# Performance work log

Measured on AMD Instinct MI355X. Metric: run time of the kernel, lower is better.

## Reference

```python
import jax, jax.numpy as jnp
import numpy as np

# pywt db2 decomposition filters
DEC_LO = np.array([-0.12940952255092145, 0.22414386804185735,
                   0.8365163037378079, 0.4829629131445341], dtype=np.float32)
DEC_HI = np.array([-0.4829629131445341, 0.8365163037378079,
                   -0.22414386804185735, -0.12940952255092145], dtype=np.float32)
LEVEL = 3
REC_WEIGHT = 1.0
FILT_LEN = 4
PAD = (2 * FILT_LEN - 3) // 2  # = 2, ptwt reflect padding per side


def _filters(dtype):
    # ptwt uses cross-correlation with flipped pywt filters (== true convolution)
    lo = jnp.asarray(DEC_LO[::-1].copy(), dtype=dtype)
    hi = jnp.asarray(DEC_HI[::-1].copy(), dtype=dtype)
    ll = jnp.outer(lo, lo)  # 'a'
    lh = jnp.outer(hi, lo)  # 'h'
    hl = jnp.outer(lo, hi)  # 'v'
    hh = jnp.outer(hi, hi)  # 'd'
    return jnp.stack([ll, lh, hl, hh])[:, None]  # [4,1,4,4]


def _dwt_step(x, filt):
    # x: [N, nb, H, W] -> [N, 4*nb, H', W'] (each band split into a,h,v,d; grouped)
    n, nb, h, w = x.shape
    padb = PAD + (h % 2)
    padr = PAD + (w % 2)
    xp = jnp.pad(x, ((0, 0), (0, 0), (PAD, padb), (PAD, padr)), mode='reflect')
    k = jnp.tile(filt, (nb, 1, 1, 1))  # [4*nb, 1, 4, 4]
    return jax.lax.conv_general_dilated(
        xp, k, window_strides=(2, 2), padding='VALID',
        feature_group_count=nb,
        dimension_numbers=('NCHW', 'OIHW', 'NCHW'))


def setup_inputs() -> dict:
    key = jax.random.key(0)
    k1, k2 = jax.random.split(key)
    preds = jax.random.normal(k1, (64, 3, 512, 512), dtype=jnp.float32)
    targets = jax.random.normal(k2, (64, 3, 512, 512), dtype=jnp.float32)
    return {"preds": preds, "targets": targets}


def reference(preds, targets):
    n, c, h, w = preds.shape
    p = preds.reshape(n * c, 1, h, w)
    t = targets.reshape(n * c, 1, h, w)
    filt = _filters(preds.dtype)
    for _ in range(LEVEL):
        p = _dwt_step(p, filt)
        t = _dwt_step(t, filt)
    # p, t: [N*C, 4**LEVEL, h', w']; leaf 0 is the all-'a' (pure approx) packet
    per_leaf_mse = jnp.mean((p - t) ** 2, axis=(0, 2, 3))  # [4**LEVEL]
    wvec = jnp.ones(per_leaf_mse.shape[0], dtype=preds.dtype).at[0].set(0.5)
    return REC_WEIGHT * jnp.dot(wvec, per_leaf_mse)
```

## Files before the change

kernel.cpp:

```cpp
#include <hip/hip_runtime.h>

#define F_LO0 0.4829629131445341f
#define F_LO1 0.8365163037378079f
#define F_LO2 0.22414386804185735f
#define F_LO3 (-0.12940952255092145f)
#define F_HI0 (-0.12940952255092145f)
#define F_HI1 (-0.22414386804185735f)
#define F_HI2 0.8365163037378079f
#define F_HI3 (-0.4829629131445341f)

__device__ __forceinline__ int reflect_idx(int r, int n) {
    r = (r < 0) ? -r : r;
    r = (r >= n) ? 2 * n - 2 - r : r;
    return r;
}

__device__ __forceinline__ float4 vfilt(const float4 a, const float4 b,
                                        const float4 c, const float4 d,
                                        float c0, float c1, float c2, float c3) {
    return make_float4(c0 * a.x + c1 * b.x + c2 * c.x + c3 * d.x,
                       c0 * a.y + c1 * b.y + c2 * c.y + c3 * d.y,
                       c0 * a.z + c1 * b.z + c2 * c.z + c3 * d.z,
                       c0 * a.w + c1 * b.w + c2 * c.w + c3 * d.w);
}

__global__ void __launch_bounds__(512, 6) k_wpt_fused(
    const float* __restrict__ p, const float* __restrict__ t,
    float* __restrict__ partial) {
    constexpr int N0 = 512, N1 = 257, N2 = 130, N3 = 66;

    __shared__ __align__(16) float sA[6080];
    __shared__ __align__(16) float sB[6912];
    __shared__ float wsum[8];

    int bid = blockIdx.x;
    int swz = (bid & 7) * (int)(gridDim.x >> 3) + (bid >> 3);
    int img = swz / 81;
    int tt = swz - img * 81;
    int TA = (tt / 9) * 8;
    int TB = (tt % 9) * 8;

    const int tid = threadIdx.x;
    const size_t ibase = (size_t)img * (N0 * N0);

    const int O0r = 8 * TA - 14, O0c = 8 * TB - 16;
    const int O1r = 4 * TA - 6, O1c = 4 * TB - 6;
    const int O2r = 2 * TA - 2, O2c = 2 * TB - 2;
    const bool edge = (TA == 0) || (TA == 64) || (TB == 0) || (TB == 64);

    if (tid < 390) {
        unsigned ru = (unsigned)tid / 5u;
        const int r = (int)ru;
        const int k = tid - (int)(5u * ru);
        const int grr = reflect_idx(O0r + r, N0);
        const float* __restrict__ prow = p + ibase + (size_t)grr * N0;
        const float* __restrict__ trow = t + ibase + (size_t)grr * N0;
        const int gc0 = O0c + 16 * k;
        float v[20];
        if ((unsigned)gc0 <= 492u) {
#pragma unroll
            for (int q = 0; q < 5; ++q) {
                const float4 pv = *(const float4*)(prow + gc0 + 4 * q);
                const float4 tv = *(const float4*)(trow + gc0 + 4 * q);
                v[4 * q + 0] = pv.x - tv.x;
                v[4 * q + 1] = pv.y - tv.y;
                v[4 * q + 2] = pv.z - tv.z;
                v[4 * q + 3] = pv.w - tv.w;
            }
        } else {
#pragma unroll
            for (int x = 0; x < 20; ++x) {
                int gc = reflect_idx(gc0 + x, N0);
                v[x] = prow[gc] - trow[gc];
            }
        }
        float* dst = sB + r * 40 + 8 * k;
        *(float4*)(dst) = make_float4(
            F_LO0 * v[2] + F_LO1 * v[3] + F_LO2 * v[4] + F_LO3 * v[5],
            F_LO0 * v[4] + F_LO1 * v[5] + F_LO2 * v[6] + F_LO3 * v[7],
            F_LO0 * v[6] + F_LO1 * v[7] + F_LO2 * v[8] + F_LO3 * v[9],
            F_LO0 * v[8] + F_LO1 * v[9] + F_LO2 * v[10] + F_LO3 * v[11]);
        *(float4*)(dst + 4) = make_float4(
            F_LO0 * v[10] + F_LO1 * v[11] + F_LO2 * v[12] + F_LO3 * v[13],
            F_LO0 * v[12] + F_LO1 * v[13] + F_LO2 * v[14] + F_LO3 * v[15],
            F_LO0 * v[14] + F_LO1 * v[15] + F_LO2 * v[16] + F_LO3 * v[17],
            F_LO0 * v[16] + F_LO1 * v[17] + F_LO2 * v[18] + F_LO3 * v[19]);
        *(float4*)(dst + 3120) = make_float4(
            F_HI0 * v[2] + F_HI1 * v[3] + F_HI2 * v[4] + F_HI3 * v[5],
            F_HI0 * v[4] + F_HI1 * v[5] + F_HI2 * v[6] + F_HI3 * v[7],
            F_HI0 * v[6] + F_HI1 * v[7] + F_HI2 * v[8] + F_HI3 * v[9],
            F_HI0 * v[8] + F_HI1 * v[9] + F_HI2 * v[10] + F_HI3 * v[11]);
        *(float4*)(dst + 3124) = make_float4(
            F_HI0 * v[10] + F_HI1 * v[11] + F_HI2 * v[12] + F_HI3 * v[13],
            F_HI0 * v[12] + F_HI1 * v[13] + F_HI2 * v[14] + F_HI3 * v[15],
            F_HI0 * v[14] + F_HI1 * v[15] + F_HI2 * v[16] + F_HI3 * v[17],
            F_HI0 * v[16] + F_HI1 * v[17] + F_HI2 * v[18] + F_HI3 * v[19]);
    }
    __syncthreads();

    if (tid < 380) {
        int r1 = tid / 10, k = tid - r1 * 10;
        const float* blo = sB + (2 * r1) * 40 + 4 * k;
        const float* bhi = blo + 3120;
        float4 L0 = *(const float4*)(blo);
        float4 L1v = *(const float4*)(blo + 40);
        float4 L2v = *(const float4*)(blo + 80);
        float4 L3v = *(const float4*)(blo + 120);
        float4 H0 = *(const float4*)(bhi);
        float4 H1 = *(const float4*)(bhi + 40);
        float4 H2 = *(const float4*)(bhi + 80);
        float4 H3 = *(const float4*)(bhi + 120);
        float4 b0 = vfilt(L0, L1v, L2v, L3v, F_LO0, F_LO1, F_LO2, F_LO3);
        float4 b1 = vfilt(L0, L1v, L2v, L3v, F_HI0, F_HI1, F_HI2, F_HI3);
        float4 b2 = vfilt(H0, H1, H2, H3, F_LO0, F_LO1, F_LO2, F_LO3);
        float4 b3 = vfilt(H0, H1, H2, H3, F_HI0, F_HI1, F_HI2, F_HI3);
        int wo = r1 * 40 + 4 * k;
        *(float4*)(sA + wo) = b0;
        *(float4*)(sA + 1520 + wo) = b1;
        *(float4*)(sA + 3040 + wo) = b2;
        *(float4*)(sA + 4560 + wo) = b3;
    }
    __syncthreads();
    if (edge) {
#pragma unroll
        for (int it = 0; it < 3; ++it) {
            int e = it * 512 + tid;
            if (e < 1444) {
                int lr = e / 38, lc = e - lr * 38;
                int sr = reflect_idx(O1r + lr, N1) - O1r;
                int sc = reflect_idx(O1c + lc, N1) - O1c;
                if ((sr != lr || sc != lc) && (unsigned)sr < 38u && (unsigned)sc < 38u) {
                    int da = lr * 40 + lc;
                    int sa = sr * 40 + sc;
                    sA[da] = sA[sa];
                    sA[1520 + da] = sA[1520 + sa];
                    sA[3040 + da] = sA[3040 + sa];
                    sA[4560 + da] = sA[4560 + sa];
                }
            }
        }
        __syncthreads();
    }

    const int w = tid >> 6;
    const int ln = tid & 63;
    const int bnd = w >> 1;
    const int hf = w & 1;
    const int off = hf * 6;
    float* scr = sB + w * 864;
    const float* L1b = sA + bnd * 1520;

    if (ln < 54) {
        const int c = ln % 18, s = ln / 18;
#pragma unroll
        for (int tq = 0; tq < 4; ++tq) {
            const int r2l = 3 * tq + s;
            const float* base = L1b + (2 * (off + r2l)) * 40 + 2 * c;
            float lo[4], hi[4];
#pragma unroll
            for (int u = 0; u < 4; ++u) {
                float2 a = *(const float2*)(base + u * 40);
                float2 d = *(const float2*)(base + u * 40 + 2);
                lo[u] = F_LO0 * a.x + F_LO1 * a.y + F_LO2 * d.x + F_LO3 * d.y;
                hi[u] = F_HI0 * a.x + F_HI1 * a.y + F_HI2 * d.x + F_HI3 * d.y;
            }
            int sl = r2l * 18 + c;
            scr[sl]       = F_LO0 * lo[0] + F_LO1 * lo[1] + F_LO2 * lo[2] + F_LO3 * lo[3];
            scr[sl + 216] = F_HI0 * lo[0] + F_HI1 * lo[1] + F_HI2 * lo[2] + F_HI3 * lo[3];
            scr[sl + 432] = F_LO0 * hi[0] + F_LO1 * hi[1] + F_LO2 * hi[2] + F_LO3 * hi[3];
            scr[sl + 648] = F_HI0 * hi[0] + F_HI1 * hi[1] + F_HI2 * hi[2] + F_HI3 * hi[3];
        }
    }

    if (edge) {
#pragma unroll
        for (int q = 0; q < 4; ++q) {
            int e = q * 54 + ln;
            if (ln < 54 && e < 216) {
                int lr = e / 18, lc = e - lr * 18;
                int srt = reflect_idx(O2r + off + lr, N2) - O2r - off;
                int sct = reflect_idx(O2c + lc, N2) - O2c;
                if ((srt != lr || sct != lc) &&
                    (unsigned)srt < 12u && (unsigned)sct < 18u) {
                    int d = lr * 18 + lc, sidx = srt * 18 + sct;
#pragma unroll
                    for (int pl = 0; pl < 4; ++pl)
                        scr[d + 216 * pl] = scr[sidx + 216 * pl];
                }
            }
        }
    }

    float local = 0.f;
    {
        const int pp = ln >> 5, rem = ln & 31, r3 = rem >> 3, j = rem & 7;
        const int i = hf * 4 + r3;
        const int sr0 = 2 * r3 + hf * 2;
        const bool valid = (TA + i < N3) && (TB + j < N3);
#pragma unroll
        for (int pi = 0; pi < 2; ++pi) {
            const int pl = 2 * pp + pi;
            const float* pb = scr + pl * 216 + sr0 * 18 + 2 * j;
            float lo[4], hi[4];
#pragma unroll
            for (int u = 0; u < 4; ++u) {
                float2 a = *(const float2*)(pb + u * 18);
                float2 d = *(const float2*)(pb + u * 18 + 2);
                lo[u] = F_LO0 * a.x + F_LO1 * a.y + F_LO2 * d.x + F_LO3 * d.y;
                hi[u] = F_HI0 * a.x + F_HI1 * a.y + F_HI2 * d.x + F_HI3 * d.y;
            }
            float o0 = F_LO0 * lo[0] + F_LO1 * lo[1] + F_LO2 * lo[2] + F_LO3 * lo[3];
            float o1 = F_HI0 * lo[0] + F_HI1 * lo[1] + F_HI2 * lo[2] + F_HI3 * lo[3];
            float o2 = F_LO0 * hi[0] + F_LO1 * hi[1] + F_LO2 * hi[2] + F_LO3 * hi[3];
            float o3 = F_HI0 * hi[0] + F_HI1 * hi[1] + F_HI2 * hi[2] + F_HI3 * hi[3];
            if (valid) {
                float w00 = (bnd == 0 && pl == 0) ? 0.5f : 1.0f;
                local += w00 * o0 * o0 + o1 * o1 + o2 * o2 + o3 * o3;
            }
        }
    }

#pragma unroll
    for (int o = 32; o > 0; o >>= 1) local += __shfl_down(local, o, 64);
    if (ln == 0) wsum[w] = local;
    __syncthreads();
    if (tid == 0) {
        float ssum = 0.f;
#pragma unroll
        for (int x = 0; x < 8; ++x) ssum += wsum[x];
        partial[blockIdx.x] = ssum;
    }
}

__global__ void __launch_bounds__(1024) k_reduce(const float* __restrict__ part,
                                                 float* __restrict__ out,
                                                 int n4, float inv_den) {
    const int tid = threadIdx.x;
    float s = 0.f;
    const float4* p4 = (const float4*)part;
    for (int i = tid; i < n4; i += 1024) {
        float4 v = p4[i];
        s += v.x + v.y + v.z + v.w;
    }
#pragma unroll
    for (int o = 32; o > 0; o >>= 1) s += __shfl_down(s, o, 64);
    __shared__ float ws_[16];
    int w = tid >> 6;
    if ((tid & 63) == 0) ws_[w] = s;
    __syncthreads();
    if (tid == 0) {
        float tot = 0.f;
#pragma unroll
        for (int i = 0; i < 16; ++i) tot += ws_[i];
        out[0] = tot * inv_den;
    }
}

extern "C" void kernel_launch(void* const* d_in, const int* in_sizes, int n_in,
                              void* d_out, int out_size, void* d_ws, size_t ws_size,
                              hipStream_t stream) {
    const float* preds = (const float*)d_in[0];
    const float* targets = (const float*)d_in[1];
    float* out = (float*)d_out;
    float* partial = (float*)d_ws;

    const float inv_den = 1.0f / (192.0f * 66.0f * 66.0f);
    const int nblk = 192 * 9 * 9;

    k_wpt_fused<<<dim3(nblk), dim3(512), 0, stream>>>(preds, targets, partial);
    k_reduce<<<dim3(1), dim3(1024), 0, stream>>>(partial, out, nblk / 4, inv_den);
}
```

Before: 205.2 us.

## Fuse level-1 row/column filtering from global memory and halve LDS scratch

```diff
diff --git a/kernel.cpp b/kernel.cpp
--- a/kernel.cpp
+++ b/kernel.cpp
@@ -15,22 +15,13 @@
     return r;
 }
 
-__device__ __forceinline__ float4 vfilt(const float4 a, const float4 b,
-                                        const float4 c, const float4 d,
-                                        float c0, float c1, float c2, float c3) {
-    return make_float4(c0 * a.x + c1 * b.x + c2 * c.x + c3 * d.x,
-                       c0 * a.y + c1 * b.y + c2 * c.y + c3 * d.y,
-                       c0 * a.z + c1 * b.z + c2 * c.z + c3 * d.z,
-                       c0 * a.w + c1 * b.w + c2 * c.w + c3 * d.w);
-}
-
-__global__ void __launch_bounds__(512, 6) k_wpt_fused(
+__global__ void __launch_bounds__(512, 8) k_wpt_fused(
     const float* __restrict__ p, const float* __restrict__ t,
     float* __restrict__ partial) {
     constexpr int N0 = 512, N1 = 257, N2 = 130, N3 = 66;
 
     __shared__ __align__(16) float sA[6080];
-    __shared__ __align__(16) float sB[6912];
+    __shared__ __align__(16) float sB[3456];
     __shared__ float wsum[8];
 
     int bid = blockIdx.x;
@@ -48,77 +39,59 @@
     const int O2r = 2 * TA - 2, O2c = 2 * TB - 2;
     const bool edge = (TA == 0) || (TA == 64) || (TB == 0) || (TB == 64);
 
-    if (tid < 390) {
-        unsigned ru = (unsigned)tid / 5u;
-        const int r = (int)ru;
-        const int k = tid - (int)(5u * ru);
-        const int grr = reflect_idx(O0r + r, N0);
-        const float* __restrict__ prow = p + ibase + (size_t)grr * N0;
-        const float* __restrict__ trow = t + ibase + (size_t)grr * N0;
-        const int gc0 = O0c + 16 * k;
-        float v[20];
-        if ((unsigned)gc0 <= 492u) {
-#pragma unroll
-            for (int q = 0; q < 5; ++q) {
-                const float4 pv = *(const float4*)(prow + gc0 + 4 * q);
-                const float4 tv = *(const float4*)(trow + gc0 + 4 * q);
-                v[4 * q + 0] = pv.x - tv.x;
-                v[4 * q + 1] = pv.y - tv.y;
-                v[4 * q + 2] = pv.z - tv.z;
-                v[4 * q + 3] = pv.w - tv.w;
-            }
-        } else {
-#pragma unroll
-            for (int x = 0; x < 20; ++x) {
-                int gc = reflect_idx(gc0 + x, N0);
-                v[x] = prow[gc] - trow[gc];
-            }
-        }
-        float* dst = sB + r * 40 + 8 * k;
-        *(float4*)(dst) = make_float4(
-            F_LO0 * v[2] + F_LO1 * v[3] + F_LO2 * v[4] + F_LO3 * v[5],
-            F_LO0 * v[4] + F_LO1 * v[5] + F_LO2 * v[6] + F_LO3 * v[7],
-            F_LO0 * v[6] + F_LO1 * v[7] + F_LO2 * v[8] + F_LO3 * v[9],
-            F_LO0 * v[8] + F_LO1 * v[9] + F_LO2 * v[10] + F_LO3 * v[11]);
-        *(float4*)(dst + 4) = make_float4(
-            F_LO0 * v[10] + F_LO1 * v[11] + F_LO2 * v[12] + F_LO3 * v[13],
-            F_LO0 * v[12] + F_LO1 * v[13] + F_LO2 * v[14] + F_LO3 * v[15],
-            F_LO0 * v[14] + F_LO1 * v[15] + F_LO2 * v[16] + F_LO3 * v[17],
-            F_LO0 * v[16] + F_LO1 * v[17] + F_LO2 * v[18] + F_LO3 * v[19]);
-        *(float4*)(dst + 3120) = make_float4(
-            F_HI0 * v[2] + F_HI1 * v[3] + F_HI2 * v[4] + F_HI3 * v[5],
-            F_HI0 * v[4] + F_HI1 * v[5] + F_HI2 * v[6] + F_HI3 * v[7],
-            F_HI0 * v[6] + F_HI1 * v[7] + F_HI2 * v[8] + F_HI3 * v[9],
-            F_HI0 * v[8] + F_HI1 * v[9] + F_HI2 * v[10] + F_HI3 * v[11]);
-        *(float4*)(dst + 3124) = make_float4(
-            F_HI0 * v[10] + F_HI1 * v[11] + F_HI2 * v[12] + F_HI3 * v[13],
-            F_HI0 * v[12] + F_HI1 * v[13] + F_HI2 * v[14] + F_HI3 * v[15],
-            F_HI0 * v[14] + F_HI1 * v[15] + F_HI2 * v[16] + F_HI3 * v[17],
-            F_HI0 * v[16] + F_HI1 * v[17] + F_HI2 * v[18] + F_HI3 * v[19]);
-    }
-    __syncthreads();
-
     if (tid < 380) {
-        int r1 = tid / 10, k = tid - r1 * 10;
-        const float* blo = sB + (2 * r1) * 40 + 4 * k;
-        const float* bhi = blo + 3120;
-        float4 L0 = *(const float4*)(blo);
-        float4 L1v = *(const float4*)(blo + 40);
-        float4 L2v = *(const float4*)(blo + 80);
-        float4 L3v = *(const float4*)(blo + 120);
-        float4 H0 = *(const float4*)(bhi);
-        float4 H1 = *(const float4*)(bhi + 40);
-        float4 H2 = *(const float4*)(bhi + 80);
-        float4 H3 = *(const float4*)(bhi + 120);
-        float4 b0 = vfilt(L0, L1v, L2v, L3v, F_LO0, F_LO1, F_LO2, F_LO3);
-        float4 b1 = vfilt(L0, L1v, L2v, L3v, F_HI0, F_HI1, F_HI2, F_HI3);
-        float4 b2 = vfilt(H0, H1, H2, H3, F_LO0, F_LO1, F_LO2, F_LO3);
-        float4 b3 = vfilt(H0, H1, H2, H3, F_HI0, F_HI1, F_HI2, F_HI3);
-        int wo = r1 * 40 + 4 * k;
-        *(float4*)(sA + wo) = b0;
-        *(float4*)(sA + 1520 + wo) = b1;
-        *(float4*)(sA + 3040 + wo) = b2;
-        *(float4*)(sA + 4560 + wo) = b3;
+        const int r1 = tid / 10, k = tid - (tid / 10) * 10;
+        const int A = O0c + 8 * k;
+        const bool vec = ((unsigned)A <= 504u);
+        const int q2 = (A <= 500) ? 8 : 4;
+        float b0[4] = {0.f, 0.f, 0.f, 0.f}, b1[4] = {0.f, 0.f, 0.f, 0.f};
+        float b2[4] = {0.f, 0.f, 0.f, 0.f}, b3[4] = {0.f, 0.f, 0.f, 0.f};
+#pragma unroll
+        for (int u = 0; u < 4; ++u) {
+            const int gr = reflect_idx(O0r + 2 * r1 + u, N0);
+            const float* __restrict__ pr = p + ibase + (size_t)gr * N0;
+            const float* __restrict__ tr = t + ibase + (size_t)gr * N0;
+            float v[12];
+            if (vec) {
+                const float4 p0 = *(const float4*)(pr + A);
+                const float4 p1 = *(const float4*)(pr + A + 4);
+                const float4 p2 = *(const float4*)(pr + A + q2);
+                const float4 t0 = *(const float4*)(tr + A);
+                const float4 t1 = *(const float4*)(tr + A + 4);
+                const float4 t2 = *(const float4*)(tr + A + q2);
+                v[0] = p0.x - t0.x; v[1] = p0.y - t0.y; v[2] = p0.z - t0.z; v[3] = p0.w - t0.w;
+                v[4] = p1.x - t1.x; v[5] = p1.y - t1.y; v[6] = p1.z - t1.z; v[7] = p1.w - t1.w;
+                v[8] = p2.x - t2.x; v[9] = p2.y - t2.y; v[10] = p2.z - t2.z; v[11] = p2.w - t2.w;
+            } else {
+#pragma unroll
+                for (int x = 0; x < 12; ++x) {
+                    int gc = reflect_idx(A + x, N0);
+                    v[x] = pr[gc] - tr[gc];
+                }
+            }
+            float lo[4], hi[4];
+#pragma unroll
+            for (int d = 0; d < 4; ++d) {
+                lo[d] = F_LO0 * v[2 * d + 2] + F_LO1 * v[2 * d + 3] +
+                        F_LO2 * v[2 * d + 4] + F_LO3 * v[2 * d + 5];
+                hi[d] = F_HI0 * v[2 * d + 2] + F_HI1 * v[2 * d + 3] +
+                        F_HI2 * v[2 * d + 4] + F_HI3 * v[2 * d + 5];
+            }
+            const float cl = (u == 0) ? F_LO0 : (u == 1) ? F_LO1 : (u == 2) ? F_LO2 : F_LO3;
+            const float ch = (u == 0) ? F_HI0 : (u == 1) ? F_HI1 : (u == 2) ? F_HI2 : F_HI3;
+#pragma unroll
+            for (int d = 0; d < 4; ++d) {
+                b0[d] += cl * lo[d];
+                b1[d] += ch * lo[d];
+                b2[d] += cl * hi[d];
+                b3[d] += ch * hi[d];
+            }
+        }
+        const int wo = r1 * 40 + 4 * k;
+        *(float4*)(sA + wo) = make_float4(b0[0], b0[1], b0[2], b0[3]);
+        *(float4*)(sA + 1520 + wo) = make_float4(b1[0], b1[1], b1[2], b1[3]);
+        *(float4*)(sA + 3040 + wo) = make_float4(b2[0], b2[1], b2[2], b2[3]);
+        *(float4*)(sA + 4560 + wo) = make_float4(b3[0], b3[1], b3[2], b3[3]);
     }
     __syncthreads();
     if (edge) {
@@ -147,60 +120,55 @@
     const int bnd = w >> 1;
     const int hf = w & 1;
     const int off = hf * 6;
-    float* scr = sB + w * 864;
+    float* scr = sB + w * 432;
     const float* L1b = sA + bnd * 1520;
 
-    if (ln < 54) {
-        const int c = ln % 18, s = ln / 18;
-#pragma unroll
-        for (int tq = 0; tq < 4; ++tq) {
-            const int r2l = 3 * tq + s;
-            const float* base = L1b + (2 * (off + r2l)) * 40 + 2 * c;
-            float lo[4], hi[4];
-#pragma unroll
-            for (int u = 0; u < 4; ++u) {
-                float2 a = *(const float2*)(base + u * 40);
-                float2 d = *(const float2*)(base + u * 40 + 2);
-                lo[u] = F_LO0 * a.x + F_LO1 * a.y + F_LO2 * d.x + F_LO3 * d.y;
-                hi[u] = F_HI0 * a.x + F_HI1 * a.y + F_HI2 * d.x + F_HI3 * d.y;
-            }
-            int sl = r2l * 18 + c;
-            scr[sl]       = F_LO0 * lo[0] + F_LO1 * lo[1] + F_LO2 * lo[2] + F_LO3 * lo[3];
-            scr[sl + 216] = F_HI0 * lo[0] + F_HI1 * lo[1] + F_HI2 * lo[2] + F_HI3 * lo[3];
-            scr[sl + 432] = F_LO0 * hi[0] + F_LO1 * hi[1] + F_LO2 * hi[2] + F_LO3 * hi[3];
-            scr[sl + 648] = F_HI0 * hi[0] + F_HI1 * hi[1] + F_HI2 * hi[2] + F_HI3 * hi[3];
-        }
-    }
-
-    if (edge) {
-#pragma unroll
-        for (int q = 0; q < 4; ++q) {
-            int e = q * 54 + ln;
-            if (ln < 54 && e < 216) {
-                int lr = e / 18, lc = e - lr * 18;
-                int srt = reflect_idx(O2r + off + lr, N2) - O2r - off;
-                int sct = reflect_idx(O2c + lc, N2) - O2c;
-                if ((srt != lr || sct != lc) &&
-                    (unsigned)srt < 12u && (unsigned)sct < 18u) {
-                    int d = lr * 18 + lc, sidx = srt * 18 + sct;
-#pragma unroll
-                    for (int pl = 0; pl < 4; ++pl)
-                        scr[d + 216 * pl] = scr[sidx + 216 * pl];
-                }
-            }
-        }
-    }
-
     float local = 0.f;
-    {
-        const int pp = ln >> 5, rem = ln & 31, r3 = rem >> 3, j = rem & 7;
-        const int i = hf * 4 + r3;
-        const int sr0 = 2 * r3 + hf * 2;
-        const bool valid = (TA + i < N3) && (TB + j < N3);
-#pragma unroll
-        for (int pi = 0; pi < 2; ++pi) {
-            const int pl = 2 * pp + pi;
-            const float* pb = scr + pl * 216 + sr0 * 18 + 2 * j;
+#pragma unroll
+    for (int pass = 0; pass < 2; ++pass) {
+        if (ln < 54) {
+            const int c = ln % 18, s = ln / 18;
+#pragma unroll
+            for (int tq = 0; tq < 4; ++tq) {
+                const int r2l = 3 * tq + s;
+                const float* base = L1b + (2 * (off + r2l)) * 40 + 2 * c;
+                float f[4];
+#pragma unroll
+                for (int u = 0; u < 4; ++u) {
+                    float2 a = *(const float2*)(base + u * 40);
+                    float2 d = *(const float2*)(base + u * 40 + 2);
+                    f[u] = (pass == 0)
+                        ? F_LO0 * a.x + F_LO1 * a.y + F_LO2 * d.x + F_LO3 * d.y
+                        : F_HI0 * a.x + F_HI1 * a.y + F_HI2 * d.x + F_HI3 * d.y;
+                }
+                int sl = r2l * 18 + c;
+                scr[sl]       = F_LO0 * f[0] + F_LO1 * f[1] + F_LO2 * f[2] + F_LO3 * f[3];
+                scr[sl + 216] = F_HI0 * f[0] + F_HI1 * f[1] + F_HI2 * f[2] + F_HI3 * f[3];
+            }
+        }
+        if (edge) {
+#pragma unroll
+            for (int q = 0; q < 4; ++q) {
+                int e = q * 54 + ln;
+                if (ln < 54 && e < 216) {
+                    int lr = e / 18, lc = e - lr * 18;
+                    int srt = reflect_idx(O2r + off + lr, N2) - O2r - off;
+                    int sct = reflect_idx(O2c + lc, N2) - O2c;
+                    if ((srt != lr || sct != lc) &&
+                        (unsigned)srt < 12u && (unsigned)sct < 18u) {
+                        int d = lr * 18 + lc, sidx = srt * 18 + sct;
+                        scr[d] = scr[sidx];
+                        scr[d + 216] = scr[sidx + 216];
+                    }
+                }
+            }
+        }
+        {
+            const int pp = ln >> 5, rem = ln & 31, r3 = rem >> 3, j = rem & 7;
+            const int i = hf * 4 + r3;
+            const int sr0 = 2 * r3 + hf * 2;
+            const bool valid = (TA + i < N3) && (TB + j < N3);
+            const float* pb = scr + pp * 216 + sr0 * 18 + 2 * j;
             float lo[4], hi[4];
 #pragma unroll
             for (int u = 0; u < 4; ++u) {
@@ -214,7 +182,7 @@
             float o2 = F_LO0 * hi[0] + F_LO1 * hi[1] + F_LO2 * hi[2] + F_LO3 * hi[3];
             float o3 = F_HI0 * hi[0] + F_HI1 * hi[1] + F_HI2 * hi[2] + F_HI3 * hi[3];
             if (valid) {
-                float w00 = (bnd == 0 && pl == 0) ? 0.5f : 1.0f;
+                float w00 = (bnd == 0 && pass == 0 && pp == 0) ? 0.5f : 1.0f;
                 local += w00 * o0 * o0 + o1 * o1 + o2 * o2 + o3 * o3;
             }
         }
```

Result: slower. 560.7 us (+173.3%).

## Convert fused wavelet kernel to persistent blocks with register prefetch of next tile

Applied to the files above, without the earlier changes.

```diff
diff --git a/kernel.cpp b/kernel.cpp
--- a/kernel.cpp
+++ b/kernel.cpp
@@ -15,6 +15,12 @@
     return r;
 }
 
+#define BARRIER()                                              \
+    do {                                                       \
+        asm volatile("s_waitcnt lgkmcnt(0)" ::: "memory");     \
+        __builtin_amdgcn_s_barrier();                          \
+    } while (0)
+
 __device__ __forceinline__ float4 vfilt(const float4 a, const float4 b,
                                         const float4 c, const float4 d,
                                         float c0, float c1, float c2, float c3) {
@@ -24,7 +30,7 @@
                        c0 * a.w + c1 * b.w + c2 * c.w + c3 * d.w);
 }
 
-__global__ void __launch_bounds__(512, 6) k_wpt_fused(
+__global__ void __launch_bounds__(512) k_wpt_persist(
     const float* __restrict__ p, const float* __restrict__ t,
     float* __restrict__ partial) {
     constexpr int N0 = 512, N1 = 257, N2 = 130, N3 = 66;
@@ -33,191 +39,210 @@
     __shared__ __align__(16) float sB[6912];
     __shared__ float wsum[8];
 
-    int bid = blockIdx.x;
-    int swz = (bid & 7) * (int)(gridDim.x >> 3) + (bid >> 3);
-    int img = swz / 81;
-    int tt = swz - img * 81;
-    int TA = (tt / 9) * 8;
-    int TB = (tt % 9) * 8;
+    const int b = blockIdx.x;
+    const int g0 = b * 30 + ((b < 192) ? b : 192);
+    const int cnt = 30 + ((b < 192) ? 1 : 0);
 
     const int tid = threadIdx.x;
-    const size_t ibase = (size_t)img * (N0 * N0);
-
-    const int O0r = 8 * TA - 14, O0c = 8 * TB - 16;
-    const int O1r = 4 * TA - 6, O1c = 4 * TB - 6;
-    const int O2r = 2 * TA - 2, O2c = 2 * TB - 2;
-    const bool edge = (TA == 0) || (TA == 64) || (TB == 0) || (TB == 64);
-
-    if (tid < 390) {
-        unsigned ru = (unsigned)tid / 5u;
-        const int r = (int)ru;
-        const int k = tid - (int)(5u * ru);
-        const int grr = reflect_idx(O0r + r, N0);
-        const float* __restrict__ prow = p + ibase + (size_t)grr * N0;
-        const float* __restrict__ trow = t + ibase + (size_t)grr * N0;
-        const int gc0 = O0c + 16 * k;
-        float v[20];
+    const int hr = tid / 5, hk = tid - (tid / 5) * 5;
+
+    float4 P[5], T[5];
+
+    auto prefetch = [&](int g) {
+        int img = g / 81;
+        int tt = g - img * 81;
+        int TAn = (tt / 9) * 8;
+        int TBn = (tt - (tt / 9) * 9) * 8;
+        int O0rn = 8 * TAn - 14, O0cn = 8 * TBn - 16;
+        int grr = reflect_idx(O0rn + hr, N0);
+        const float* __restrict__ prow = p + (size_t)img * (N0 * N0) + (size_t)grr * N0;
+        const float* __restrict__ trow = t + (size_t)img * (N0 * N0) + (size_t)grr * N0;
+        int gc0 = O0cn + 16 * hk;
         if ((unsigned)gc0 <= 492u) {
 #pragma unroll
             for (int q = 0; q < 5; ++q) {
-                const float4 pv = *(const float4*)(prow + gc0 + 4 * q);
-                const float4 tv = *(const float4*)(trow + gc0 + 4 * q);
-                v[4 * q + 0] = pv.x - tv.x;
-                v[4 * q + 1] = pv.y - tv.y;
-                v[4 * q + 2] = pv.z - tv.z;
-                v[4 * q + 3] = pv.w - tv.w;
+                P[q] = *(const float4*)(prow + gc0 + 4 * q);
+                T[q] = *(const float4*)(trow + gc0 + 4 * q);
             }
         } else {
 #pragma unroll
-            for (int x = 0; x < 20; ++x) {
-                int gc = reflect_idx(gc0 + x, N0);
-                v[x] = prow[gc] - trow[gc];
-            }
-        }
-        float* dst = sB + r * 40 + 8 * k;
-        *(float4*)(dst) = make_float4(
-            F_LO0 * v[2] + F_LO1 * v[3] + F_LO2 * v[4] + F_LO3 * v[5],
-            F_LO0 * v[4] + F_LO1 * v[5] + F_LO2 * v[6] + F_LO3 * v[7],
-            F_LO0 * v[6] + F_LO1 * v[7] + F_LO2 * v[8] + F_LO3 * v[9],
-            F_LO0 * v[8] + F_LO1 * v[9] + F_LO2 * v[10] + F_LO3 * v[11]);
-        *(float4*)(dst + 4) = make_float4(
-            F_LO0 * v[10] + F_LO1 * v[11] + F_LO2 * v[12] + F_LO3 * v[13],
-            F_LO0 * v[12] + F_LO1 * v[13] + F_LO2 * v[14] + F_LO3 * v[15],
-            F_LO0 * v[14] + F_LO1 * v[15] + F_LO2 * v[16] + F_LO3 * v[17],
-            F_LO0 * v[16] + F_LO1 * v[17] + F_LO2 * v[18] + F_LO3 * v[19]);
-        *(float4*)(dst + 3120) = make_float4(
-            F_HI0 * v[2] + F_HI1 * v[3] + F_HI2 * v[4] + F_HI3 * v[5],
-            F_HI0 * v[4] + F_HI1 * v[5] + F_HI2 * v[6] + F_HI3 * v[7],
-            F_HI0 * v[6] + F_HI1 * v[7] + F_HI2 * v[8] + F_HI3 * v[9],
-            F_HI0 * v[8] + F_HI1 * v[9] + F_HI2 * v[10] + F_HI3 * v[11]);
-        *(float4*)(dst + 3124) = make_float4(
-            F_HI0 * v[10] + F_HI1 * v[11] + F_HI2 * v[12] + F_HI3 * v[13],
-            F_HI0 * v[12] + F_HI1 * v[13] + F_HI2 * v[14] + F_HI3 * v[15],
-            F_HI0 * v[14] + F_HI1 * v[15] + F_HI2 * v[16] + F_HI3 * v[17],
-            F_HI0 * v[16] + F_HI1 * v[17] + F_HI2 * v[18] + F_HI3 * v[19]);
-    }
-    __syncthreads();
-
-    if (tid < 380) {
-        int r1 = tid / 10, k = tid - r1 * 10;
-        const float* blo = sB + (2 * r1) * 40 + 4 * k;
-        const float* bhi = blo + 3120;
-        float4 L0 = *(const float4*)(blo);
-        float4 L1v = *(const float4*)(blo + 40);
-        float4 L2v = *(const float4*)(blo + 80);
-        float4 L3v = *(const float4*)(blo + 120);
-        float4 H0 = *(const float4*)(bhi);
-        float4 H1 = *(const float4*)(bhi + 40);
-        float4 H2 = *(const float4*)(bhi + 80);
-        float4 H3 = *(const float4*)(bhi + 120);
-        float4 b0 = vfilt(L0, L1v, L2v, L3v, F_LO0, F_LO1, F_LO2, F_LO3);
-        float4 b1 = vfilt(L0, L1v, L2v, L3v, F_HI0, F_HI1, F_HI2, F_HI3);
-        float4 b2 = vfilt(H0, H1, H2, H3, F_LO0, F_LO1, F_LO2, F_LO3);
-        float4 b3 = vfilt(H0, H1, H2, H3, F_HI0, F_HI1, F_HI2, F_HI3);
-        int wo = r1 * 40 + 4 * k;
-        *(float4*)(sA + wo) = b0;
-        *(float4*)(sA + 1520 + wo) = b1;
-        *(float4*)(sA + 3040 + wo) = b2;
-        *(float4*)(sA + 4560 + wo) = b3;
-    }
-    __syncthreads();
-    if (edge) {
-#pragma unroll
-        for (int it = 0; it < 3; ++it) {
-            int e = it * 512 + tid;
-            if (e < 1444) {
-                int lr = e / 38, lc = e - lr * 38;
-                int sr = reflect_idx(O1r + lr, N1) - O1r;
-                int sc = reflect_idx(O1c + lc, N1) - O1c;
-                if ((sr != lr || sc != lc) && (unsigned)sr < 38u && (unsigned)sc < 38u) {
-                    int da = lr * 40 + lc;
-                    int sa = sr * 40 + sc;
-                    sA[da] = sA[sa];
-                    sA[1520 + da] = sA[1520 + sa];
-                    sA[3040 + da] = sA[3040 + sa];
-                    sA[4560 + da] = sA[4560 + sa];
-                }
-            }
-        }
-        __syncthreads();
-    }
-
+            for (int q = 0; q < 5; ++q) {
+                int c0 = reflect_idx(gc0 + 4 * q + 0, N0);
+                int c1 = reflect_idx(gc0 + 4 * q + 1, N0);
+                int c2 = reflect_idx(gc0 + 4 * q + 2, N0);
+                int c3 = reflect_idx(gc0 + 4 * q + 3, N0);
+                P[q] = make_float4(prow[c0], prow[c1], prow[c2], prow[c3]);
+                T[q] = make_float4(trow[c0], trow[c1], trow[c2], trow[c3]);
+            }
+        }
+    };
+
+    if (tid < 390) prefetch(g0);
+
+    float local = 0.f;
     const int w = tid >> 6;
     const int ln = tid & 63;
     const int bnd = w >> 1;
     const int hf = w & 1;
     const int off = hf * 6;
     float* scr = sB + w * 864;
-    const float* L1b = sA + bnd * 1520;
-
-    if (ln < 54) {
-        const int c = ln % 18, s = ln / 18;
-#pragma unroll
-        for (int tq = 0; tq < 4; ++tq) {
-            const int r2l = 3 * tq + s;
-            const float* base = L1b + (2 * (off + r2l)) * 40 + 2 * c;
-            float lo[4], hi[4];
-#pragma unroll
-            for (int u = 0; u < 4; ++u) {
-                float2 a = *(const float2*)(base + u * 40);
-                float2 d = *(const float2*)(base + u * 40 + 2);
-                lo[u] = F_LO0 * a.x + F_LO1 * a.y + F_LO2 * d.x + F_LO3 * d.y;
-                hi[u] = F_HI0 * a.x + F_HI1 * a.y + F_HI2 * d.x + F_HI3 * d.y;
-            }
-            int sl = r2l * 18 + c;
-            scr[sl]       = F_LO0 * lo[0] + F_LO1 * lo[1] + F_LO2 * lo[2] + F_LO3 * lo[3];
-            scr[sl + 216] = F_HI0 * lo[0] + F_HI1 * lo[1] + F_HI2 * lo[2] + F_HI3 * lo[3];
-            scr[sl + 432] = F_LO0 * hi[0] + F_LO1 * hi[1] + F_LO2 * hi[2] + F_LO3 * hi[3];
-            scr[sl + 648] = F_HI0 * hi[0] + F_HI1 * hi[1] + F_HI2 * hi[2] + F_HI3 * hi[3];
-        }
-    }
-
-    if (edge) {
-#pragma unroll
-        for (int q = 0; q < 4; ++q) {
-            int e = q * 54 + ln;
-            if (ln < 54 && e < 216) {
-                int lr = e / 18, lc = e - lr * 18;
-                int srt = reflect_idx(O2r + off + lr, N2) - O2r - off;
-                int sct = reflect_idx(O2c + lc, N2) - O2c;
-                if ((srt != lr || sct != lc) &&
-                    (unsigned)srt < 12u && (unsigned)sct < 18u) {
-                    int d = lr * 18 + lc, sidx = srt * 18 + sct;
-#pragma unroll
-                    for (int pl = 0; pl < 4; ++pl)
-                        scr[d + 216 * pl] = scr[sidx + 216 * pl];
-                }
-            }
-        }
-    }
-
-    float local = 0.f;
-    {
-        const int pp = ln >> 5, rem = ln & 31, r3 = rem >> 3, j = rem & 7;
-        const int i = hf * 4 + r3;
-        const int sr0 = 2 * r3 + hf * 2;
-        const bool valid = (TA + i < N3) && (TB + j < N3);
-#pragma unroll
-        for (int pi = 0; pi < 2; ++pi) {
-            const int pl = 2 * pp + pi;
-            const float* pb = scr + pl * 216 + sr0 * 18 + 2 * j;
-            float lo[4], hi[4];
-#pragma unroll
-            for (int u = 0; u < 4; ++u) {
-                float2 a = *(const float2*)(pb + u * 18);
-                float2 d = *(const float2*)(pb + u * 18 + 2);
-                lo[u] = F_LO0 * a.x + F_LO1 * a.y + F_LO2 * d.x + F_LO3 * d.y;
-                hi[u] = F_HI0 * a.x + F_HI1 * a.y + F_HI2 * d.x + F_HI3 * d.y;
-            }
-            float o0 = F_LO0 * lo[0] + F_LO1 * lo[1] + F_LO2 * lo[2] + F_LO3 * lo[3];
-            float o1 = F_HI0 * lo[0] + F_HI1 * lo[1] + F_HI2 * lo[2] + F_HI3 * lo[3];
-            float o2 = F_LO0 * hi[0] + F_LO1 * hi[1] + F_LO2 * hi[2] + F_LO3 * hi[3];
-            float o3 = F_HI0 * hi[0] + F_HI1 * hi[1] + F_HI2 * hi[2] + F_HI3 * hi[3];
-            if (valid) {
-                float w00 = (bnd == 0 && pl == 0) ? 0.5f : 1.0f;
-                local += w00 * o0 * o0 + o1 * o1 + o2 * o2 + o3 * o3;
-            }
-        }
+
+    for (int it = 0; it < cnt; ++it) {
+        const int g = g0 + it;
+        const int img = g / 81;
+        const int tt = g - img * 81;
+        const int TA = (tt / 9) * 8;
+        const int TB = (tt - (tt / 9) * 9) * 8;
+        const int O1r = 4 * TA - 6, O1c = 4 * TB - 6;
+        const int O2r = 2 * TA - 2, O2c = 2 * TB - 2;
+        const bool edge = (TA == 0) || (TA == 64) || (TB == 0) || (TB == 64);
+
+        if (tid < 390) {
+            float v[20];
+#pragma unroll
+            for (int q = 0; q < 5; ++q) {
+                v[4 * q + 0] = P[q].x - T[q].x;
+                v[4 * q + 1] = P[q].y - T[q].y;
+                v[4 * q + 2] = P[q].z - T[q].z;
+                v[4 * q + 3] = P[q].w - T[q].w;
+            }
+            if (it + 1 < cnt) prefetch(g + 1);
+            float* dst = sB + hr * 40 + 8 * hk;
+            *(float4*)(dst) = make_float4(
+                F_LO0 * v[2] + F_LO1 * v[3] + F_LO2 * v[4] + F_LO3 * v[5],
+                F_LO0 * v[4] + F_LO1 * v[5] + F_LO2 * v[6] + F_LO3 * v[7],
+                F_LO0 * v[6] + F_LO1 * v[7] + F_LO2 * v[8] + F_LO3 * v[9],
+                F_LO0 * v[8] + F_LO1 * v[9] + F_LO2 * v[10] + F_LO3 * v[11]);
+            *(float4*)(dst + 4) = make_float4(
+                F_LO0 * v[10] + F_LO1 * v[11] + F_LO2 * v[12] + F_LO3 * v[13],
+                F_LO0 * v[12] + F_LO1 * v[13] + F_LO2 * v[14] + F_LO3 * v[15],
+                F_LO0 * v[14] + F_LO1 * v[15] + F_LO2 * v[16] + F_LO3 * v[17],
+                F_LO0 * v[16] + F_LO1 * v[17] + F_LO2 * v[18] + F_LO3 * v[19]);
+            *(float4*)(dst + 3120) = make_float4(
+                F_HI0 * v[2] + F_HI1 * v[3] + F_HI2 * v[4] + F_HI3 * v[5],
+                F_HI0 * v[4] + F_HI1 * v[5] + F_HI2 * v[6] + F_HI3 * v[7],
+                F_HI0 * v[6] + F_HI1 * v[7] + F_HI2 * v[8] + F_HI3 * v[9],
+                F_HI0 * v[8] + F_HI1 * v[9] + F_HI2 * v[10] + F_HI3 * v[11]);
+            *(float4*)(dst + 3124) = make_float4(
+                F_HI0 * v[10] + F_HI1 * v[11] + F_HI2 * v[12] + F_HI3 * v[13],
+                F_HI0 * v[12] + F_HI1 * v[13] + F_HI2 * v[14] + F_HI3 * v[15],
+                F_HI0 * v[14] + F_HI1 * v[15] + F_HI2 * v[16] + F_HI3 * v[17],
+                F_HI0 * v[16] + F_HI1 * v[17] + F_HI2 * v[18] + F_HI3 * v[19]);
+        }
+        BARRIER();
+
+        if (tid < 380) {
+            int r1 = tid / 10, k = tid - (tid / 10) * 10;
+            const float* blo = sB + (2 * r1) * 40 + 4 * k;
+            const float* bhi = blo + 3120;
+            float4 L0 = *(const float4*)(blo);
+            float4 L1v = *(const float4*)(blo + 40);
+            float4 L2v = *(const float4*)(blo + 80);
+            float4 L3v = *(const float4*)(blo + 120);
+            float4 H0 = *(const float4*)(bhi);
+            float4 H1 = *(const float4*)(bhi + 40);
+            float4 H2 = *(const float4*)(bhi + 80);
+            float4 H3 = *(const float4*)(bhi + 120);
+            float4 b0 = vfilt(L0, L1v, L2v, L3v, F_LO0, F_LO1, F_LO2, F_LO3);
+            float4 b1 = vfilt(L0, L1v, L2v, L3v, F_HI0, F_HI1, F_HI2, F_HI3);
+            float4 b2 = vfilt(H0, H1, H2, H3, F_LO0, F_LO1, F_LO2, F_LO3);
+            float4 b3 = vfilt(H0, H1, H2, H3, F_HI0, F_HI1, F_HI2, F_HI3);
+            int wo = r1 * 40 + 4 * k;
+            *(float4*)(sA + wo) = b0;
+            *(float4*)(sA + 1520 + wo) = b1;
+            *(float4*)(sA + 3040 + wo) = b2;
+            *(float4*)(sA + 4560 + wo) = b3;
+        }
+        BARRIER();
+        if (edge) {
+#pragma unroll
+            for (int pit = 0; pit < 3; ++pit) {
+                int e = pit * 512 + tid;
+                if (e < 1444) {
+                    int lr = e / 38, lc = e - lr * 38;
+                    int sr = reflect_idx(O1r + lr, N1) - O1r;
+                    int sc = reflect_idx(O1c + lc, N1) - O1c;
+                    if ((sr != lr || sc != lc) && (unsigned)sr < 38u && (unsigned)sc < 38u) {
+                        int da = lr * 40 + lc;
+                        int sa = sr * 40 + sc;
+                        sA[da] = sA[sa];
+                        sA[1520 + da] = sA[1520 + sa];
+                        sA[3040 + da] = sA[3040 + sa];
+                        sA[4560 + da] = sA[4560 + sa];
+                    }
+                }
+            }
+            BARRIER();
+        }
+
+        const float* L1b = sA + bnd * 1520;
+        if (ln < 54) {
+            const int c = ln % 18, s = ln / 18;
+#pragma unroll
+            for (int tq = 0; tq < 4; ++tq) {
+                const int r2l = 3 * tq + s;
+                const float* base = L1b + (2 * (off + r2l)) * 40 + 2 * c;
+                float lo[4], hi[4];
+#pragma unroll
+                for (int u = 0; u < 4; ++u) {
+                    float2 a = *(const float2*)(base + u * 40);
+                    float2 d = *(const float2*)(base + u * 40 + 2);
+                    lo[u] = F_LO0 * a.x + F_LO1 * a.y + F_LO2 * d.x + F_LO3 * d.y;
+                    hi[u] = F_HI0 * a.x + F_HI1 * a.y + F_HI2 * d.x + F_HI3 * d.y;
+                }
+                int sl = r2l * 18 + c;
+                scr[sl]       = F_LO0 * lo[0] + F_LO1 * lo[1] + F_LO2 * lo[2] + F_LO3 * lo[3];
+                scr[sl + 216] = F_HI0 * lo[0] + F_HI1 * lo[1] + F_HI2 * lo[2] + F_HI3 * lo[3];
+                scr[sl + 432] = F_LO0 * hi[0] + F_LO1 * hi[1] + F_LO2 * hi[2] + F_LO3 * hi[3];
+                scr[sl + 648] = F_HI0 * hi[0] + F_HI1 * hi[1] + F_HI2 * hi[2] + F_HI3 * hi[3];
+            }
+        }
+        if (edge) {
+#pragma unroll
+            for (int q = 0; q < 4; ++q) {
+                int e = q * 54 + ln;
+                if (ln < 54 && e < 216) {
+                    int lr = e / 18, lc = e - lr * 18;
+                    int srt = reflect_idx(O2r + off + lr, N2) - O2r - off;
+                    int sct = reflect_idx(O2c + lc, N2) - O2c;
+                    if ((srt != lr || sct != lc) &&
+                        (unsigned)srt < 12u && (unsigned)sct < 18u) {
+                        int d = lr * 18 + lc, sidx = srt * 18 + sct;
+#pragma unroll
+                        for (int pl = 0; pl < 4; ++pl)
+                            scr[d + 216 * pl] = scr[sidx + 216 * pl];
+                    }
+                }
+            }
+        }
+        {
+            const int pp = ln >> 5, rem = ln & 31, r3 = rem >> 3, j = rem & 7;
+            const int i = hf * 4 + r3;
+            const int sr0 = 2 * r3 + hf * 2;
+            const bool valid = (TA + i < N3) && (TB + j < N3);
+#pragma unroll
+            for (int pi = 0; pi < 2; ++pi) {
+                const int pl = 2 * pp + pi;
+                const float* pb = scr + pl * 216 + sr0 * 18 + 2 * j;
+                float lo[4], hi[4];
+#pragma unroll
+                for (int u = 0; u < 4; ++u) {
+                    float2 a = *(const float2*)(pb + u * 18);
+                    float2 d = *(const float2*)(pb + u * 18 + 2);
+                    lo[u] = F_LO0 * a.x + F_LO1 * a.y + F_LO2 * d.x + F_LO3 * d.y;
+                    hi[u] = F_HI0 * a.x + F_HI1 * a.y + F_HI2 * d.x + F_HI3 * d.y;
+                }
+                float o0 = F_LO0 * lo[0] + F_LO1 * lo[1] + F_LO2 * lo[2] + F_LO3 * lo[3];
+                float o1 = F_HI0 * lo[0] + F_HI1 * lo[1] + F_HI2 * lo[2] + F_HI3 * lo[3];
+                float o2 = F_LO0 * hi[0] + F_LO1 * hi[1] + F_LO2 * hi[2] + F_LO3 * hi[3];
+                float o3 = F_HI0 * hi[0] + F_HI1 * hi[1] + F_HI2 * hi[2] + F_HI3 * hi[3];
+                if (valid) {
+                    float w00 = (bnd == 0 && pl == 0) ? 0.5f : 1.0f;
+                    local += w00 * o0 * o0 + o1 * o1 + o2 * o2 + o3 * o3;
+                }
+            }
+        }
+        BARRIER();
     }
 
 #pragma unroll
@@ -228,30 +253,25 @@
         float ssum = 0.f;
 #pragma unroll
         for (int x = 0; x < 8; ++x) ssum += wsum[x];
-        partial[blockIdx.x] = ssum;
+        partial[b] = ssum;
     }
 }
 
-__global__ void __launch_bounds__(1024) k_reduce(const float* __restrict__ part,
-                                                 float* __restrict__ out,
-                                                 int n4, float inv_den) {
+__global__ void __launch_bounds__(512) k_reduce(const float* __restrict__ part,
+                                                float* __restrict__ out,
+                                                float inv_den) {
     const int tid = threadIdx.x;
-    float s = 0.f;
-    const float4* p4 = (const float4*)part;
-    for (int i = tid; i < n4; i += 1024) {
-        float4 v = p4[i];
-        s += v.x + v.y + v.z + v.w;
-    }
+    float s = part[tid];
 #pragma unroll
     for (int o = 32; o > 0; o >>= 1) s += __shfl_down(s, o, 64);
-    __shared__ float ws_[16];
+    __shared__ float ws_[8];
     int w = tid >> 6;
     if ((tid & 63) == 0) ws_[w] = s;
     __syncthreads();
     if (tid == 0) {
         float tot = 0.f;
 #pragma unroll
-        for (int i = 0; i < 16; ++i) tot += ws_[i];
+        for (int i = 0; i < 8; ++i) tot += ws_[i];
         out[0] = tot * inv_den;
     }
 }
@@ -265,8 +285,7 @@
     float* partial = (float*)d_ws;
 
     const float inv_den = 1.0f / (192.0f * 66.0f * 66.0f);
-    const int nblk = 192 * 9 * 9;
-
-    k_wpt_fused<<<dim3(nblk), dim3(512), 0, stream>>>(preds, targets, partial);
-    k_reduce<<<dim3(1), dim3(1024), 0, stream>>>(partial, out, nblk / 4, inv_den);
-}
+
+    k_wpt_persist<<<dim3(512), dim3(512), 0, stream>>>(preds, targets, partial);
+    k_reduce<<<dim3(1), dim3(512), 0, stream>>>(partial, out, inv_den);
+}
```

Measured after the change: 346.5 us. +68.8%, slower.

## Compute level-2 tile once per block in shared memory instead of per-wave halves

Applied to the files above, without the earlier changes.

```diff
diff --git a/kernel.cpp b/kernel.cpp
--- a/kernel.cpp
+++ b/kernel.cpp
@@ -24,13 +24,13 @@
                        c0 * a.w + c1 * b.w + c2 * c.w + c3 * d.w);
 }
 
-__global__ void __launch_bounds__(512, 6) k_wpt_fused(
+__global__ void __launch_bounds__(512) k_wpt_fused(
     const float* __restrict__ p, const float* __restrict__ t,
     float* __restrict__ partial) {
     constexpr int N0 = 512, N1 = 257, N2 = 130, N3 = 66;
 
     __shared__ __align__(16) float sA[6080];
-    __shared__ __align__(16) float sB[6912];
+    __shared__ __align__(16) float sB[6240];
     __shared__ float wsum[8];
 
     int bid = blockIdx.x;
@@ -99,7 +99,7 @@
     __syncthreads();
 
     if (tid < 380) {
-        int r1 = tid / 10, k = tid - r1 * 10;
+        int r1 = tid / 10, k = tid - (tid / 10) * 10;
         const float* blo = sB + (2 * r1) * 40 + 4 * k;
         const float* bhi = blo + 3120;
         float4 L0 = *(const float4*)(blo);
@@ -142,20 +142,12 @@
         __syncthreads();
     }
 
-    const int w = tid >> 6;
-    const int ln = tid & 63;
-    const int bnd = w >> 1;
-    const int hf = w & 1;
-    const int off = hf * 6;
-    float* scr = sB + w * 864;
-    const float* L1b = sA + bnd * 1520;
-
-    if (ln < 54) {
-        const int c = ln % 18, s = ln / 18;
-#pragma unroll
-        for (int tq = 0; tq < 4; ++tq) {
-            const int r2l = 3 * tq + s;
-            const float* base = L1b + (2 * (off + r2l)) * 40 + 2 * c;
+    if (tid < 324) {
+        const int r2 = tid / 18, c2 = tid - 18 * r2;
+        const int rb = r2 * 80 + 2 * c2;
+#pragma unroll
+        for (int b = 0; b < 4; ++b) {
+            const float* base = sA + b * 1520 + rb;
             float lo[4], hi[4];
 #pragma unroll
             for (int u = 0; u < 4; ++u) {
@@ -164,43 +156,39 @@
                 lo[u] = F_LO0 * a.x + F_LO1 * a.y + F_LO2 * d.x + F_LO3 * d.y;
                 hi[u] = F_HI0 * a.x + F_HI1 * a.y + F_HI2 * d.x + F_HI3 * d.y;
             }
-            int sl = r2l * 18 + c;
-            scr[sl]       = F_LO0 * lo[0] + F_LO1 * lo[1] + F_LO2 * lo[2] + F_LO3 * lo[3];
-            scr[sl + 216] = F_HI0 * lo[0] + F_HI1 * lo[1] + F_HI2 * lo[2] + F_HI3 * lo[3];
-            scr[sl + 432] = F_LO0 * hi[0] + F_LO1 * hi[1] + F_LO2 * hi[2] + F_LO3 * hi[3];
-            scr[sl + 648] = F_HI0 * hi[0] + F_HI1 * hi[1] + F_HI2 * hi[2] + F_HI3 * hi[3];
-        }
-    }
-
+            float* dst = sB + (b * 4) * 324 + tid;
+            dst[0]       = F_LO0 * lo[0] + F_LO1 * lo[1] + F_LO2 * lo[2] + F_LO3 * lo[3];
+            dst[324]     = F_HI0 * lo[0] + F_HI1 * lo[1] + F_HI2 * lo[2] + F_HI3 * lo[3];
+            dst[648]     = F_LO0 * hi[0] + F_LO1 * hi[1] + F_LO2 * hi[2] + F_LO3 * hi[3];
+            dst[972]     = F_HI0 * hi[0] + F_HI1 * hi[1] + F_HI2 * hi[2] + F_HI3 * hi[3];
+        }
+    }
+    __syncthreads();
     if (edge) {
-#pragma unroll
-        for (int q = 0; q < 4; ++q) {
-            int e = q * 54 + ln;
-            if (ln < 54 && e < 216) {
-                int lr = e / 18, lc = e - lr * 18;
-                int srt = reflect_idx(O2r + off + lr, N2) - O2r - off;
-                int sct = reflect_idx(O2c + lc, N2) - O2c;
-                if ((srt != lr || sct != lc) &&
-                    (unsigned)srt < 12u && (unsigned)sct < 18u) {
-                    int d = lr * 18 + lc, sidx = srt * 18 + sct;
-#pragma unroll
-                    for (int pl = 0; pl < 4; ++pl)
-                        scr[d + 216 * pl] = scr[sidx + 216 * pl];
-                }
-            }
-        }
+        if (tid < 324) {
+            const int lr = tid / 18, lc = tid - 18 * lr;
+            int sr = reflect_idx(O2r + lr, N2) - O2r;
+            int sc = reflect_idx(O2c + lc, N2) - O2c;
+            if ((sr != lr || sc != lc) && (unsigned)sr < 18u && (unsigned)sc < 18u) {
+                int d = lr * 18 + lc;
+                int s = sr * 18 + sc;
+#pragma unroll
+                for (int pl = 0; pl < 16; ++pl) sB[pl * 324 + d] = sB[pl * 324 + s];
+            }
+        }
+        __syncthreads();
     }
 
     float local = 0.f;
     {
-        const int pp = ln >> 5, rem = ln & 31, r3 = rem >> 3, j = rem & 7;
-        const int i = hf * 4 + r3;
-        const int sr0 = 2 * r3 + hf * 2;
+        const int pos = tid & 63;
+        const int i = pos >> 3, j = pos & 7;
         const bool valid = (TA + i < N3) && (TB + j < N3);
-#pragma unroll
-        for (int pi = 0; pi < 2; ++pi) {
-            const int pl = 2 * pp + pi;
-            const float* pb = scr + pl * 216 + sr0 * 18 + 2 * j;
+        const int cell = (2 * i) * 18 + 2 * j;
+#pragma unroll
+        for (int q = 0; q < 2; ++q) {
+            const int pl = (tid >> 6) + 8 * q;
+            const float* pb = sB + pl * 324 + cell;
             float lo[4], hi[4];
 #pragma unroll
             for (int u = 0; u < 4; ++u) {
@@ -214,7 +202,7 @@
             float o2 = F_LO0 * hi[0] + F_LO1 * hi[1] + F_LO2 * hi[2] + F_LO3 * hi[3];
             float o3 = F_HI0 * hi[0] + F_HI1 * hi[1] + F_HI2 * hi[2] + F_HI3 * hi[3];
             if (valid) {
-                float w00 = (bnd == 0 && pl == 0) ? 0.5f : 1.0f;
+                float w00 = (pl == 0) ? 0.5f : 1.0f;
                 local += w00 * o0 * o0 + o1 * o1 + o2 * o2 + o3 * o3;
             }
         }
@@ -222,7 +210,8 @@
 
 #pragma unroll
     for (int o = 32; o > 0; o >>= 1) local += __shfl_down(local, o, 64);
-    if (ln == 0) wsum[w] = local;
+    const int w = tid >> 6;
+    if ((tid & 63) == 0) wsum[w] = local;
     __syncthreads();
     if (tid == 0) {
         float ssum = 0.f;
```

Measured after the change: 202.3 us. About the same (-1.4%).
